# Performance work log

Hardware: AMD Instinct MI355X
Metric: run time of the kernel (lower is better)

## Reference

```python
import jax, jax.numpy as jnp
import numpy as np

E = 12000          # edge_num
D = 49 * 128       # sphere_basis_reduce * sphere_channels_reduce
H = 256            # hidden_channel
C = 128            # sphere_channels_reduce


def setup_inputs() -> dict:
    key = jax.random.key(0)
    ks = jax.random.split(key, 7)
    scale1 = 1.0 / np.sqrt(D)
    scale2 = 1.0 / np.sqrt(H)
    return {
        "node_embed": jax.random.normal(ks[0], (E, D), jnp.float32),
        "x_edge_c": jax.random.normal(ks[1], (E, H), jnp.float32),
        "ori": jax.random.normal(ks[2], (E, D), jnp.float32),
        "W1": jax.random.normal(ks[3], (D, H), jnp.float32) * scale1,
        "b1": jax.random.normal(ks[4], (H,), jnp.float32) * scale1,
        "W2": jax.random.normal(ks[5], (H, D), jnp.float32) * scale2,
        "b2": jax.random.normal(ks[6], (D,), jnp.float32) * scale2,
        "edge_num": E,
    }


def reference(node_embed, x_edge_c, ori, W1, b1, W2, b2, edge_num):
    # cat along edge axis: [2E, D]
    x = jnp.concatenate([node_embed, ori], axis=0)
    # fc1 + SiLU: [2E, H]
    h = jax.nn.silu(x @ W1 + b1)
    # edge-gated multiply, x_edge_c broadcast across the 2-way cat axis
    h = (h.reshape(2, edge_num, H) * x_edge_c.reshape(1, edge_num, H)).reshape(-1, H)
    # fc2 + SiLU: [2E, D]
    y = jax.nn.silu(h @ W2 + b2)
    # split-and-add combine: [E, D/C, C]
    y = y.reshape(2 * edge_num, -1, C)
    return y[:edge_num] + y[edge_num:]
```

## Files before the change

### kernel.cpp

```cpp
#include <hip/hip_runtime.h>

#define E_NUM 12000
#define D_DIM 6272
#define H_DIM 256
#define M1 24000

typedef __attribute__((ext_vector_type(8))) short short8;
typedef __attribute__((ext_vector_type(8))) __bf16 bf16x8;
typedef __attribute__((ext_vector_type(4))) float f32x4;

__device__ __forceinline__ float silu_f(float x) {
  return x / (1.0f + __expf(-x));
}

__device__ __forceinline__ bf16x8 ld_frag(const short* p) {
  return __builtin_bit_cast(bf16x8, *(const short8*)p);
}

__device__ __forceinline__ bf16x8 cvt8(f32x4 a, f32x4 b) {
  bf16x8 r;
#pragma unroll
  for (int j = 0; j < 4; ++j) {
    r[j] = (__bf16)a[j];
    r[4 + j] = (__bf16)b[j];
  }
  return r;
}

__device__ __forceinline__ void gll16(const void* g, void* l) {
  __builtin_amdgcn_global_load_lds(
      (const __attribute__((address_space(1))) void*)g,
      (__attribute__((address_space(3))) void*)l, 16, 0, 0);
}

__global__ void pack_p1(const float* __restrict__ W1, short* __restrict__ P1) {
  const int kt = blockIdx.x;
  const int col = threadIdx.x;
  const float* src = W1 + (size_t)kt * 32 * H_DIM + col;
  short* dst = P1 + ((size_t)kt * H_DIM + col) * 32;
#pragma unroll
  for (int c = 0; c < 4; ++c) {
    short8 s;
#pragma unroll
    for (int j = 0; j < 8; ++j)
      s[j] = __builtin_bit_cast(short, (__bf16)src[(size_t)(c * 8 + j) * H_DIM]);
    *(short8*)(dst + c * 8) = s;
  }
}

__global__ void pack_p2(const float* __restrict__ W2, short* __restrict__ P2) {
  const int kt = blockIdx.y;
  const int col = blockIdx.x * 128 + threadIdx.x;
  const float* src = W2 + (size_t)kt * 32 * D_DIM + col;
  short* dst = P2 + ((size_t)kt * D_DIM + col) * 32;
#pragma unroll
  for (int c = 0; c < 4; ++c) {
    short8 s;
#pragma unroll
    for (int j = 0; j < 8; ++j)
      s[j] = __builtin_bit_cast(short, (__bf16)src[(size_t)(c * 8 + j) * D_DIM]);
    *(short8*)(dst + c * 8) = s;
  }
}

#define G1_ST 98
__launch_bounds__(256, 3)
__global__ void gemm1_kernel(const float* __restrict__ node_embed,
                             const float* __restrict__ ori,
                             const float* __restrict__ x_edge_c,
                             const short* __restrict__ P1,
                             const float* __restrict__ b1,
                             short* __restrict__ hgp) {
  __shared__ __align__(16) float Als[2][32 * 64];

  const int t = threadIdx.x;
  const int wn = t >> 6;
  const int lane = t & 63;
  const int l15 = lane & 15;
  const int lq = lane >> 4;
  const int m_base = blockIdx.x * 32;

  const float* xb = (m_base < E_NUM) ? (node_embed + (size_t)m_base * D_DIM)
                                     : (ori + (size_t)(m_base - E_NUM) * D_DIM);

  const int R0 = t >> 4;
  const int cst = t & 15;
  const int cl = ((((cst >> 1) ^ (R0 & 7)) << 1) | (cst & 1));
  const float* asrc0 = xb + (size_t)R0 * D_DIM + cl * 4;
  const float* asrc1 = xb + (size_t)(R0 + 16) * D_DIM + cl * 4;

  const short* bbase = P1 + (size_t)(wn * 64 + l15) * 32 + lq * 8;

  const int asw = l15 & 7;

  f32x4 acc[2][4];
#pragma unroll
  for (int m = 0; m < 2; ++m)
#pragma unroll
    for (int n = 0; n < 4; ++n) acc[m][n] = (f32x4){0.f, 0.f, 0.f, 0.f};

  gll16(asrc0, &Als[0][t * 4]);
  gll16(asrc1, &Als[0][t * 4 + 1024]);
  __syncthreads();

  int cur = 0;
  for (int it = 0; it < G1_ST; ++it) {
    const int nxt = cur ^ 1;
    if (it + 1 < G1_ST) {
      const size_t ko = (size_t)(it + 1) * 64;
      gll16(asrc0 + ko, &Als[nxt][t * 4]);
      gll16(asrc1 + ko, &Als[nxt][t * 4 + 1024]);
    }
    bf16x8 bq[2][4];
    {
      const short* bs = bbase + (size_t)it * 16384;
#pragma unroll
      for (int ks = 0; ks < 2; ++ks)
#pragma unroll
        for (int n = 0; n < 4; ++n) bq[ks][n] = ld_frag(bs + ks * 8192 + n * 512);
    }
    bf16x8 af[2][2];
    {
      const float* Ac = &Als[cur][0];
#pragma unroll
      for (int m = 0; m < 2; ++m)
#pragma unroll
        for (int ks = 0; ks < 2; ++ks) {
          const int fidx = (m * 16 + l15) * 64 + (((ks * 4 + lq) ^ asw) * 8);
          f32x4 lo = *(const f32x4*)(Ac + fidx);
          f32x4 hi = *(const f32x4*)(Ac + fidx + 4);
          af[m][ks] = cvt8(lo, hi);
        }
    }
#pragma unroll
    for (int ks = 0; ks < 2; ++ks)
#pragma unroll
      for (int m = 0; m < 2; ++m)
#pragma unroll
        for (int n = 0; n < 4; ++n)
          acc[m][n] = __builtin_amdgcn_mfma_f32_16x16x32_bf16(af[m][ks], bq[ks][n],
                                                              acc[m][n], 0, 0, 0);
    __syncthreads();
    cur = nxt;
  }

#pragma unroll
  for (int n = 0; n < 4; ++n) {
    const int col = wn * 64 + n * 16 + l15;
    const float b1v = b1[col];
    const int panel = wn * 2 + (n >> 1);
    const int cin = (n & 1) * 16 + l15;
#pragma unroll
    for (int m = 0; m < 2; ++m) {
#pragma unroll
      for (int i = 0; i < 4; ++i) {
        const int gmr = m_base + m * 16 + lq * 4 + i;
        const int e = (gmr < E_NUM) ? gmr : gmr - E_NUM;
        float v = acc[m][n][i] + b1v;
        v = silu_f(v) * x_edge_c[(size_t)e * H_DIM + col];
        hgp[((size_t)panel * M1 + gmr) * 32 + cin] = __builtin_bit_cast(short, (__bf16)v);
      }
    }
  }
}

__launch_bounds__(256, 3)
__global__ void gemm2_kernel(const short* __restrict__ hgp,
                             const short* __restrict__ P2,
                             const float* __restrict__ b2,
                             float* __restrict__ out) {
  __shared__ __align__(16) short Als[2][128 * 64];

  const int t = threadIdx.x;
  const int wave = t >> 6;
  const int lane = t & 63;
  const int l15 = lane & 15;
  const int lq = lane >> 4;
  const int wr = wave >> 1;
  const int wc = wave & 1;
  const int d0 = blockIdx.x * 128;
  const int e0 = blockIdx.y * 64;

  const int R0 = t >> 3;
  const int cst = t & 7;
  const int cl = cst ^ (R0 & 7);
  const short* asrc[4];
#pragma unroll
  for (int r = 0; r < 4; ++r) {
    int er = e0 + R0 + (r & 1) * 32;
    if (er >= E_NUM) er = E_NUM - 1;
    const int grow = er + (r >> 1) * E_NUM;
    asrc[r] = hgp + (size_t)(cl >> 2) * (M1 * 32) + (size_t)grow * 32 + (cl & 3) * 8;
  }

  const short* bbase = P2 + (size_t)(d0 + wc * 64 + l15) * 32 + lq * 8;
  const int asw = l15 & 7;

  f32x4 acc[2][2][4];
#pragma unroll
  for (int h = 0; h < 2; ++h)
#pragma unroll
    for (int m = 0; m < 2; ++m)
#pragma unroll
      for (int n = 0; n < 4; ++n) acc[h][m][n] = (f32x4){0.f, 0.f, 0.f, 0.f};

#pragma unroll
  for (int r = 0; r < 4; ++r) gll16(asrc[r], &Als[0][t * 8 + r * 2048]);
  __syncthreads();

  int cur = 0;
#pragma unroll
  for (int it = 0; it < 4; ++it) {
    const int nxt = cur ^ 1;
    if (it < 3) {
      const size_t ko = (size_t)(it + 1) * 2 * (M1 * 32);
#pragma unroll
      for (int r = 0; r < 4; ++r) gll16(asrc[r] + ko, &Als[nxt][t * 8 + r * 2048]);
    }
    bf16x8 bq[2][4];
#pragma unroll
    for (int ks = 0; ks < 2; ++ks)
#pragma unroll
      for (int n = 0; n < 4; ++n)
        bq[ks][n] = ld_frag(bbase + (size_t)(it * 2 + ks) * (D_DIM * 32) + n * 512);

    bf16x8 af[2][2][2];
#pragma unroll
    for (int h = 0; h < 2; ++h)
#pragma unroll
      for (int m = 0; m < 2; ++m)
#pragma unroll
        for (int ks = 0; ks < 2; ++ks) {
          const int R = h * 64 + wr * 32 + m * 16 + l15;
          af[h][m][ks] = ld_frag(&Als[cur][R * 64 + (((ks * 4 + lq) ^ asw) * 8)]);
        }
#pragma unroll
    for (int ks = 0; ks < 2; ++ks)
#pragma unroll
      for (int h = 0; h < 2; ++h)
#pragma unroll
        for (int m = 0; m < 2; ++m)
#pragma unroll
          for (int n = 0; n < 4; ++n)
            acc[h][m][n] = __builtin_amdgcn_mfma_f32_16x16x32_bf16(
                af[h][m][ks], bq[ks][n], acc[h][m][n], 0, 0, 0);
    __syncthreads();
    cur = nxt;
  }

#pragma unroll
  for (int n = 0; n < 4; ++n) {
    const int col = d0 + wc * 64 + n * 16 + l15;
    const float b2v = b2[col];
#pragma unroll
    for (int m = 0; m < 2; ++m) {
#pragma unroll
      for (int i = 0; i < 4; ++i) {
        const int e = e0 + wr * 32 + m * 16 + lq * 4 + i;
        if (e < E_NUM) {
          out[(size_t)e * D_DIM + col] =
              silu_f(acc[0][m][n][i] + b2v) + silu_f(acc[1][m][n][i] + b2v);
        }
      }
    }
  }
}

extern "C" void kernel_launch(void* const* d_in, const int* in_sizes, int n_in,
                              void* d_out, int out_size, void* d_ws, size_t ws_size,
                              hipStream_t stream) {
  const float* node_embed = (const float*)d_in[0];
  const float* x_edge_c = (const float*)d_in[1];
  const float* ori = (const float*)d_in[2];
  const float* W1 = (const float*)d_in[3];
  const float* b1 = (const float*)d_in[4];
  const float* W2 = (const float*)d_in[5];
  const float* b2 = (const float*)d_in[6];
  float* out_p = (float*)d_out;

  char* ws = (char*)d_ws;
  short* P1 = (short*)ws;
  short* P2 = (short*)(ws + 3211264);
  short* hgp = (short*)(ws + 2 * 3211264);

  pack_p1<<<dim3(D_DIM / 32), 256, 0, stream>>>(W1, P1);
  pack_p2<<<dim3(D_DIM / 128, 8), 128, 0, stream>>>(W2, P2);

  gemm1_kernel<<<dim3(M1 / 32), 256, 0, stream>>>(node_embed, ori, x_edge_c, P1, b1, hgp);

  gemm2_kernel<<<dim3(D_DIM / 128, (E_NUM + 63) / 64), 256, 0, stream>>>(hgp, P2, b2, out_p);
}
```

Baseline: 436.2 us.

## Stage weight tiles in LDS and enlarge GEMM1 M-tile to 64 rows

GEMM1 now processes 64 rows per block with a K-step of 32, and loads the packed W1 tile into shared memory with async global-to-LDS copies instead of having each wave read B fragments straight from global memory. GEMM2 likewise stages both the gated-hidden A tile and the W2 B tile in swizzled LDS with K-step 32 and 8 iterations, and raises the occupancy hint to 4. The aim is to cut redundant global or L2 weight traffic and to overlap the weight loads with MFMA work. In exchange it uses more LDS per block, doubles the number of loop iterations and barriers, and halves GEMM1's grid size.

```diff
diff --git a/kernel.cpp b/kernel.cpp
--- a/kernel.cpp
+++ b/kernel.cpp
@@ -63,7 +63,7 @@
   }
 }
 
-#define G1_ST 98
+#define G1_IT 196
 __launch_bounds__(256, 3)
 __global__ void gemm1_kernel(const float* __restrict__ node_embed,
                              const float* __restrict__ ori,
@@ -71,75 +71,77 @@
                              const short* __restrict__ P1,
                              const float* __restrict__ b1,
                              short* __restrict__ hgp) {
-  __shared__ __align__(16) float Als[2][32 * 64];
+  __shared__ __align__(16) float Als[2][64 * 32];
+  __shared__ __align__(16) short Bls[2][256 * 32];
 
   const int t = threadIdx.x;
   const int wn = t >> 6;
   const int lane = t & 63;
   const int l15 = lane & 15;
   const int lq = lane >> 4;
-  const int m_base = blockIdx.x * 32;
-
-  const float* xb = (m_base < E_NUM) ? (node_embed + (size_t)m_base * D_DIM)
-                                     : (ori + (size_t)(m_base - E_NUM) * D_DIM);
-
-  const int R0 = t >> 4;
-  const int cst = t & 15;
-  const int cl = ((((cst >> 1) ^ (R0 & 7)) << 1) | (cst & 1));
-  const float* asrc0 = xb + (size_t)R0 * D_DIM + cl * 4;
-  const float* asrc1 = xb + (size_t)(R0 + 16) * D_DIM + cl * 4;
-
-  const short* bbase = P1 + (size_t)(wn * 64 + l15) * 32 + lq * 8;
-
-  const int asw = l15 & 7;
-
-  f32x4 acc[2][4];
-#pragma unroll
-  for (int m = 0; m < 2; ++m)
+  const int m_base = blockIdx.x * 64;
+
+  const int sr = t >> 3;
+  const int sgl = ((t >> 1) & 3) ^ (sr & 3);
+  const int grow0 = m_base + sr;
+  const int grow1 = m_base + sr + 32;
+  const float* aAsrc = ((grow0 < E_NUM) ? node_embed + (size_t)grow0 * D_DIM
+                                        : ori + (size_t)(grow0 - E_NUM) * D_DIM) +
+                       sgl * 8 + (t & 1) * 4;
+  const float* aBsrc = ((grow1 < E_NUM) ? node_embed + (size_t)grow1 * D_DIM
+                                        : ori + (size_t)(grow1 - E_NUM) * D_DIM) +
+                       sgl * 8 + (t & 1) * 4;
+
+  const int bct = t >> 2;
+  const int bgl = (t & 3) ^ (bct & 3);
+  const short* bsrc = P1 + (size_t)bct * 32 + bgl * 8;
+
+  const int axor = l15 & 3;
+
+  f32x4 acc[4][4];
+#pragma unroll
+  for (int m = 0; m < 4; ++m)
 #pragma unroll
     for (int n = 0; n < 4; ++n) acc[m][n] = (f32x4){0.f, 0.f, 0.f, 0.f};
 
-  gll16(asrc0, &Als[0][t * 4]);
-  gll16(asrc1, &Als[0][t * 4 + 1024]);
+  gll16(aAsrc, &Als[0][t * 4]);
+  gll16(aBsrc, &Als[0][t * 4 + 1024]);
+#pragma unroll
+  for (int j = 0; j < 4; ++j) gll16(bsrc + j * 2048, &Bls[0][t * 8 + j * 2048]);
   __syncthreads();
 
   int cur = 0;
-  for (int it = 0; it < G1_ST; ++it) {
+  for (int it = 0; it < G1_IT; ++it) {
     const int nxt = cur ^ 1;
-    if (it + 1 < G1_ST) {
-      const size_t ko = (size_t)(it + 1) * 64;
-      gll16(asrc0 + ko, &Als[nxt][t * 4]);
-      gll16(asrc1 + ko, &Als[nxt][t * 4 + 1024]);
-    }
-    bf16x8 bq[2][4];
-    {
-      const short* bs = bbase + (size_t)it * 16384;
-#pragma unroll
-      for (int ks = 0; ks < 2; ++ks)
-#pragma unroll
-        for (int n = 0; n < 4; ++n) bq[ks][n] = ld_frag(bs + ks * 8192 + n * 512);
-    }
-    bf16x8 af[2][2];
+    if (it + 1 < G1_IT) {
+      const float* aa = aAsrc + (size_t)(it + 1) * 32;
+      const float* ab = aBsrc + (size_t)(it + 1) * 32;
+      gll16(aa, &Als[nxt][t * 4]);
+      gll16(ab, &Als[nxt][t * 4 + 1024]);
+      const short* bs = bsrc + (size_t)(it + 1) * 8192;
+#pragma unroll
+      for (int j = 0; j < 4; ++j) gll16(bs + j * 2048, &Bls[nxt][t * 8 + j * 2048]);
+    }
+    bf16x8 af[4];
     {
       const float* Ac = &Als[cur][0];
 #pragma unroll
-      for (int m = 0; m < 2; ++m)
-#pragma unroll
-        for (int ks = 0; ks < 2; ++ks) {
-          const int fidx = (m * 16 + l15) * 64 + (((ks * 4 + lq) ^ asw) * 8);
-          f32x4 lo = *(const f32x4*)(Ac + fidx);
-          f32x4 hi = *(const f32x4*)(Ac + fidx + 4);
-          af[m][ks] = cvt8(lo, hi);
-        }
-    }
-#pragma unroll
-    for (int ks = 0; ks < 2; ++ks)
-#pragma unroll
-      for (int m = 0; m < 2; ++m)
-#pragma unroll
-        for (int n = 0; n < 4; ++n)
-          acc[m][n] = __builtin_amdgcn_mfma_f32_16x16x32_bf16(af[m][ks], bq[ks][n],
-                                                              acc[m][n], 0, 0, 0);
+      for (int m = 0; m < 4; ++m) {
+        const int ridx = (m * 16 + l15) * 32 + ((lq ^ axor) * 8);
+        f32x4 lo = *(const f32x4*)(Ac + ridx);
+        f32x4 hi = *(const f32x4*)(Ac + ridx + 4);
+        af[m] = cvt8(lo, hi);
+      }
+    }
+    bf16x8 bq[4];
+#pragma unroll
+    for (int n = 0; n < 4; ++n)
+      bq[n] = ld_frag(&Bls[cur][(wn * 64 + n * 16 + l15) * 32 + ((lq ^ axor) * 8)]);
+#pragma unroll
+    for (int m = 0; m < 4; ++m)
+#pragma unroll
+      for (int n = 0; n < 4; ++n)
+        acc[m][n] = __builtin_amdgcn_mfma_f32_16x16x32_bf16(af[m], bq[n], acc[m][n], 0, 0, 0);
     __syncthreads();
     cur = nxt;
   }
@@ -151,7 +153,7 @@
     const int panel = wn * 2 + (n >> 1);
     const int cin = (n & 1) * 16 + l15;
 #pragma unroll
-    for (int m = 0; m < 2; ++m) {
+    for (int m = 0; m < 4; ++m) {
 #pragma unroll
       for (int i = 0; i < 4; ++i) {
         const int gmr = m_base + m * 16 + lq * 4 + i;
@@ -164,102 +166,83 @@
   }
 }
 
-__launch_bounds__(256, 3)
+__launch_bounds__(256, 4)
 __global__ void gemm2_kernel(const short* __restrict__ hgp,
                              const short* __restrict__ P2,
                              const float* __restrict__ b2,
                              float* __restrict__ out) {
-  __shared__ __align__(16) short Als[2][128 * 64];
+  __shared__ __align__(16) short Als2[2][128 * 32];
+  __shared__ __align__(16) short Bls2[2][128 * 32];
 
   const int t = threadIdx.x;
-  const int wave = t >> 6;
+  const int wd = t >> 6;
   const int lane = t & 63;
   const int l15 = lane & 15;
   const int lq = lane >> 4;
-  const int wr = wave >> 1;
-  const int wc = wave & 1;
   const int d0 = blockIdx.x * 128;
   const int e0 = blockIdx.y * 64;
 
-  const int R0 = t >> 3;
-  const int cst = t & 7;
-  const int cl = cst ^ (R0 & 7);
-  const short* asrc[4];
-#pragma unroll
-  for (int r = 0; r < 4; ++r) {
-    int er = e0 + R0 + (r & 1) * 32;
-    if (er >= E_NUM) er = E_NUM - 1;
-    const int grow = er + (r >> 1) * E_NUM;
-    asrc[r] = hgp + (size_t)(cl >> 2) * (M1 * 32) + (size_t)grow * 32 + (cl & 3) * 8;
-  }
-
-  const short* bbase = P2 + (size_t)(d0 + wc * 64 + l15) * 32 + lq * 8;
-  const int asw = l15 & 7;
-
-  f32x4 acc[2][2][4];
-#pragma unroll
-  for (int h = 0; h < 2; ++h)
-#pragma unroll
-    for (int m = 0; m < 2; ++m)
-#pragma unroll
-      for (int n = 0; n < 4; ++n) acc[h][m][n] = (f32x4){0.f, 0.f, 0.f, 0.f};
-
-#pragma unroll
-  for (int r = 0; r < 4; ++r) gll16(asrc[r], &Als[0][t * 8 + r * 2048]);
+  const int sr = t >> 2;
+  const int sgl = (t & 3) ^ (sr & 3);
+  int eA = e0 + sr;
+  if (eA >= E_NUM) eA = E_NUM - 1;
+  const short* a0src = hgp + (size_t)eA * 32 + sgl * 8;
+  const short* a1src = hgp + (size_t)(E_NUM + eA) * 32 + sgl * 8;
+  const short* bsrc = P2 + (size_t)(d0 + sr) * 32 + sgl * 8;
+
+  const int axor = l15 & 3;
+
+  f32x4 acc[8][2];
+#pragma unroll
+  for (int m = 0; m < 8; ++m)
+#pragma unroll
+    for (int n = 0; n < 2; ++n) acc[m][n] = (f32x4){0.f, 0.f, 0.f, 0.f};
+
+  gll16(a0src, &Als2[0][t * 8]);
+  gll16(a1src, &Als2[0][t * 8 + 2048]);
+  gll16(bsrc, &Bls2[0][t * 8]);
+  gll16(bsrc + 2048, &Bls2[0][t * 8 + 2048]);
   __syncthreads();
 
   int cur = 0;
 #pragma unroll
-  for (int it = 0; it < 4; ++it) {
+  for (int it = 0; it < 8; ++it) {
     const int nxt = cur ^ 1;
-    if (it < 3) {
-      const size_t ko = (size_t)(it + 1) * 2 * (M1 * 32);
-#pragma unroll
-      for (int r = 0; r < 4; ++r) gll16(asrc[r] + ko, &Als[nxt][t * 8 + r * 2048]);
-    }
-    bf16x8 bq[2][4];
-#pragma unroll
-    for (int ks = 0; ks < 2; ++ks)
-#pragma unroll
-      for (int n = 0; n < 4; ++n)
-        bq[ks][n] = ld_frag(bbase + (size_t)(it * 2 + ks) * (D_DIM * 32) + n * 512);
-
-    bf16x8 af[2][2][2];
-#pragma unroll
-    for (int h = 0; h < 2; ++h)
-#pragma unroll
-      for (int m = 0; m < 2; ++m)
-#pragma unroll
-        for (int ks = 0; ks < 2; ++ks) {
-          const int R = h * 64 + wr * 32 + m * 16 + l15;
-          af[h][m][ks] = ld_frag(&Als[cur][R * 64 + (((ks * 4 + lq) ^ asw) * 8)]);
-        }
-#pragma unroll
-    for (int ks = 0; ks < 2; ++ks)
-#pragma unroll
-      for (int h = 0; h < 2; ++h)
-#pragma unroll
-        for (int m = 0; m < 2; ++m)
-#pragma unroll
-          for (int n = 0; n < 4; ++n)
-            acc[h][m][n] = __builtin_amdgcn_mfma_f32_16x16x32_bf16(
-                af[h][m][ks], bq[ks][n], acc[h][m][n], 0, 0, 0);
+    if (it < 7) {
+      const size_t ka = (size_t)(it + 1) * (M1 * 32);
+      const size_t kb = (size_t)(it + 1) * ((size_t)D_DIM * 32);
+      gll16(a0src + ka, &Als2[nxt][t * 8]);
+      gll16(a1src + ka, &Als2[nxt][t * 8 + 2048]);
+      gll16(bsrc + kb, &Bls2[nxt][t * 8]);
+      gll16(bsrc + kb + 2048, &Bls2[nxt][t * 8 + 2048]);
+    }
+    bf16x8 bq[2];
+#pragma unroll
+    for (int n = 0; n < 2; ++n)
+      bq[n] = ld_frag(&Bls2[cur][(wd * 32 + n * 16 + l15) * 32 + ((lq ^ axor) * 8)]);
+#pragma unroll
+    for (int m = 0; m < 8; ++m) {
+      bf16x8 af = ld_frag(&Als2[cur][(m * 16 + l15) * 32 + ((lq ^ axor) * 8)]);
+#pragma unroll
+      for (int n = 0; n < 2; ++n)
+        acc[m][n] = __builtin_amdgcn_mfma_f32_16x16x32_bf16(af, bq[n], acc[m][n], 0, 0, 0);
+    }
     __syncthreads();
     cur = nxt;
   }
 
 #pragma unroll
-  for (int n = 0; n < 4; ++n) {
-    const int col = d0 + wc * 64 + n * 16 + l15;
+  for (int n = 0; n < 2; ++n) {
+    const int col = d0 + wd * 32 + n * 16 + l15;
     const float b2v = b2[col];
 #pragma unroll
-    for (int m = 0; m < 2; ++m) {
+    for (int mm = 0; mm < 4; ++mm) {
 #pragma unroll
       for (int i = 0; i < 4; ++i) {
-        const int e = e0 + wr * 32 + m * 16 + lq * 4 + i;
+        const int e = e0 + mm * 16 + lq * 4 + i;
         if (e < E_NUM) {
           out[(size_t)e * D_DIM + col] =
-              silu_f(acc[0][m][n][i] + b2v) + silu_f(acc[1][m][n][i] + b2v);
+              silu_f(acc[mm][n][i] + b2v) + silu_f(acc[mm + 4][n][i] + b2v);
         }
       }
     }
@@ -286,7 +269,7 @@
   pack_p1<<<dim3(D_DIM / 32), 256, 0, stream>>>(W1, P1);
   pack_p2<<<dim3(D_DIM / 128, 8), 128, 0, stream>>>(W2, P2);
 
-  gemm1_kernel<<<dim3(M1 / 32), 256, 0, stream>>>(node_embed, ori, x_edge_c, P1, b1, hgp);
+  gemm1_kernel<<<dim3(M1 / 64), 256, 0, stream>>>(node_embed, ori, x_edge_c, P1, b1, hgp);
 
   gemm2_kernel<<<dim3(D_DIM / 128, (E_NUM + 63) / 64), 256, 0, stream>>>(hgp, P2, b2, out_p);
 }
```

Result: slower. 507.1 us (+16.2%).
